# Kernel tuning notes

Measured on AMD Instinct MI355X. Metric: run time of the kernel, lower is better.

Reference implementation:

```python
import jax, jax.numpy as jnp
import numpy as np

EMB = 1024
HEADS = 16
HEADSIZE = EMB // HEADS
LN_EPS = 1e-5


def layernorm(x, w, b):
    # normalize over last dim (headsize)
    mu = jnp.mean(x, axis=-1, keepdims=True)
    var = jnp.var(x, axis=-1, keepdims=True)
    return (x - mu) * jax.lax.rsqrt(var + LN_EPS) * w + b


def setup_inputs() -> dict:
    key = jax.random.key(0)
    ks = jax.random.split(key, 8)
    B, S, C = 2, 2048, 2048
    x = jax.random.normal(ks[0], (B, S, EMB), dtype=jnp.float32)
    context = jax.random.normal(ks[1], (B, C, EMB), dtype=jnp.float32)
    mask = jnp.ones((B, S), dtype=jnp.float32)
    contextMask = jnp.ones((B, C), dtype=jnp.float32)
    s = 0.02
    Wq = jax.random.normal(ks[2], (EMB, EMB), dtype=jnp.float32) * s
    Wk = jax.random.normal(ks[3], (EMB, EMB), dtype=jnp.float32) * s
    Wv = jax.random.normal(ks[4], (EMB, EMB), dtype=jnp.float32) * s
    Wu = jax.random.normal(ks[5], (EMB, EMB), dtype=jnp.float32) * s
    bu = jnp.zeros((EMB,), dtype=jnp.float32)
    qln_w = jnp.ones((HEADSIZE,), dtype=jnp.float32)
    qln_b = jnp.zeros((HEADSIZE,), dtype=jnp.float32)
    kln_w = jnp.ones((HEADSIZE,), dtype=jnp.float32)
    kln_b = jnp.zeros((HEADSIZE,), dtype=jnp.float32)
    return {"x": x, "context": context, "mask": mask, "contextMask": contextMask,
            "Wq": Wq, "Wk": Wk, "Wv": Wv, "Wu": Wu, "bu": bu,
            "qln_w": qln_w, "qln_b": qln_b, "kln_w": kln_w, "kln_b": kln_b}


def reference(x, context, mask, contextMask, Wq, Wk, Wv, Wu, bu, qln_w, qln_b, kln_w, kln_b):
    B, S, E = x.shape
    C = context.shape[1]
    T = S + C
    xc = jnp.concatenate([x, context], axis=1)            # [B, T, E]
    q = (x @ Wq).reshape(B, S, HEADS, HEADSIZE)
    k = (xc @ Wk).reshape(B, T, HEADS, HEADSIZE)
    v = (xc @ Wv).reshape(B, T, HEADS, HEADSIZE)
    q = layernorm(q, qln_w, qln_b)
    k = layernorm(k, kln_w, kln_b)
    scale = E ** 0.25
    q = q / scale
    k = k / scale
    # [B, H, S, T] score matrix (explicitly materialized, as in the original)
    dot = jnp.einsum('bshd,bthd->bhst', q, k)
    mcat = jnp.concatenate([mask, contextMask], axis=1)   # [B, T]
    dotMask = mask[:, None, :, None] * mcat[:, None, None, :]  # [B,1,S,T]
    # hand-rolled masked softmax: softmax(dot*mask) * mask, renormalize
    p = jax.nn.softmax(dot * dotMask, axis=-1) * dotMask
    p = p / (jnp.sum(p, axis=-1, keepdims=True) + 1e-13)
    out = jnp.einsum('bhst,bthd->bshd', p, v).reshape(B, S, E)
    return out @ Wu + bu
```

## Files before the change

### kernel.cpp

```cpp
#include <hip/hip_runtime.h>
#include <hip/hip_bf16.h>
#include <cstdint>

#define B_SZ   2
#define S_LEN  2048
#define C_LEN  2048
#define T_LEN  4096
#define EMB_   1024
#define HEADS_ 16
#define D_     64

typedef __attribute__((ext_vector_type(8))) short bf16x8;
typedef __attribute__((ext_vector_type(4))) float f32x4;
typedef __attribute__((ext_vector_type(16))) float f32x16;
typedef __attribute__((ext_vector_type(2))) float f32x2;

__device__ __forceinline__ unsigned short f2bf(float f) {
    unsigned u = __builtin_bit_cast(unsigned, f);
    u += 0x7fffu + ((u >> 16) & 1u);
    return (unsigned short)(u >> 16);
}
__device__ __forceinline__ float bf2f(unsigned short h) {
    return __builtin_bit_cast(float, (unsigned)h << 16);
}

__global__ void build_xcb_k(const float* __restrict__ x, const float* __restrict__ ctx,
                            unsigned short* __restrict__ xcb) {
    int i = blockIdx.x * blockDim.x + threadIdx.x;
    size_t e8 = (size_t)i * 8;
    int b = (int)(e8 / ((size_t)T_LEN * EMB_));
    size_t rem = e8 % ((size_t)T_LEN * EMB_);
    int t = (int)(rem / EMB_);
    int c = (int)(rem % EMB_);
    const float* src = (t < S_LEN)
        ? &x[((size_t)b * S_LEN + t) * EMB_ + c]
        : &ctx[((size_t)b * C_LEN + (t - S_LEN)) * EMB_ + c];
    float4 v0 = ((const float4*)src)[0];
    float4 v1 = ((const float4*)src)[1];
    uint4 o;
    o.x = (unsigned)f2bf(v0.x) | ((unsigned)f2bf(v0.y) << 16);
    o.y = (unsigned)f2bf(v0.z) | ((unsigned)f2bf(v0.w) << 16);
    o.z = (unsigned)f2bf(v1.x) | ((unsigned)f2bf(v1.y) << 16);
    o.w = (unsigned)f2bf(v1.z) | ((unsigned)f2bf(v1.w) << 16);
    *(uint4*)&xcb[e8] = o;
}

__global__ void mcat_k(const float* __restrict__ mask, const float* __restrict__ cmask,
                       float* __restrict__ Mcat) {
    int i = blockIdx.x * 256 + threadIdx.x;
    int b = i / T_LEN, t = i % T_LEN;
    Mcat[i] = (t < S_LEN) ? mask[(size_t)b * S_LEN + t]
                          : cmask[(size_t)b * C_LEN + (t - S_LEN)];
}

__global__ void wtrans4_k(const float* __restrict__ W0, const float* __restrict__ W1,
                          const float* __restrict__ W2, const float* __restrict__ W3,
                          unsigned short* __restrict__ T0, unsigned short* __restrict__ T1,
                          unsigned short* __restrict__ T2, unsigned short* __restrict__ T3) {
    __shared__ __align__(16) unsigned short tile[64][72];
    int bx = blockIdx.x, by = blockIdx.y, bz = blockIdx.z;
    const float* W = (bz == 0) ? W0 : (bz == 1) ? W1 : (bz == 2) ? W2 : W3;
    unsigned short* WT = (bz == 0) ? T0 : (bz == 1) ? T1 : (bz == 2) ? T2 : T3;
    int tid = threadIdx.x;
#pragma unroll
    for (int r = 0; r < 4; ++r) {
        int idx = tid + r * 256;
        int row = idx >> 4, c4 = idx & 15;
        float4 v = ((const float4*)&W[((size_t)(by * 64 + row)) * EMB_ + bx * 64])[c4];
        tile[row][c4 * 4 + 0] = f2bf(v.x);
        tile[row][c4 * 4 + 1] = f2bf(v.y);
        tile[row][c4 * 4 + 2] = f2bf(v.z);
        tile[row][c4 * 4 + 3] = f2bf(v.w);
    }
    __syncthreads();
#pragma unroll
    for (int r = 0; r < 2; ++r) {
        int idx = tid + r * 256;
        int n = idx >> 3, k8 = idx & 7;
        uint4 o;
        unsigned q[4];
#pragma unroll
        for (int j = 0; j < 4; ++j)
            q[j] = (unsigned)tile[k8 * 8 + 2 * j][n] | ((unsigned)tile[k8 * 8 + 2 * j + 1][n] << 16);
        o.x = q[0]; o.y = q[1]; o.z = q[2]; o.w = q[3];
        *(uint4*)&WT[((size_t)(bx * 64 + n)) * EMB_ + by * 64 + k8 * 8] = o;
    }
}

__global__ __launch_bounds__(256) void gemm_qkv_k(
    const unsigned short* __restrict__ A,
    const unsigned short* __restrict__ Bt,
    unsigned short* __restrict__ Yk,
    unsigned short* __restrict__ Yv,
    unsigned short* __restrict__ Yq) {
    constexpr int KTOT = 1024, NTOT = 1024;
    int nt = blockIdx.x, mt = blockIdx.y;
    if (nt >= 16 && (mt & 31) >= 16) return;
    __shared__ __align__(16) unsigned short As[128 * 32];
    __shared__ __align__(16) unsigned short Bs[128 * 32];
    int in_row0 = mt * 128;
    unsigned short* Cout;
    int col0, out_row0;
    if (nt < 8)       { Cout = Yk; col0 = nt * 128;        out_row0 = mt * 128; }
    else if (nt < 16) { Cout = Yv; col0 = (nt - 8) * 128;  out_row0 = mt * 128; }
    else              { Cout = Yq; col0 = (nt - 16) * 128;
                        out_row0 = (mt >> 5) * 2048 + (mt & 31) * 128; }
    int tid = threadIdx.x, w = tid >> 6, l = tid & 63, l15 = l & 15, lg = l >> 4;
    int wr = (w >> 1) * 64, wc = (w & 1) * 64;

    f32x4 zero4 = {0.f, 0.f, 0.f, 0.f};
    f32x4 acc[4][4];
#pragma unroll
    for (int i = 0; i < 4; ++i)
#pragma unroll
        for (int j = 0; j < 4; ++j) acc[i][j] = zero4;

    for (int k0 = 0; k0 < KTOT; k0 += 32) {
#pragma unroll
        for (int j = 0; j < 2; ++j) {
            int o = tid * 16 + j * 4096;
            int row = o >> 6;
            int ke = (o & 63) >> 1;
            __builtin_amdgcn_global_load_lds(
                (const __attribute__((address_space(1))) void*)&A[(size_t)(in_row0 + row) * KTOT + k0 + ke],
                (__attribute__((address_space(3))) void*)&As[o >> 1], 16, 0, 0);
            __builtin_amdgcn_global_load_lds(
                (const __attribute__((address_space(1))) void*)&Bt[(size_t)(nt * 128 + row) * KTOT + k0 + ke],
                (__attribute__((address_space(3))) void*)&Bs[o >> 1], 16, 0, 0);
        }
        __syncthreads();
        bf16x8 af[4], bf[4];
#pragma unroll
        for (int fr = 0; fr < 4; ++fr)
            af[fr] = *(const bf16x8*)&As[(wr + fr * 16 + l15) * 32 + lg * 8];
#pragma unroll
        for (int fc = 0; fc < 4; ++fc)
            bf[fc] = *(const bf16x8*)&Bs[(wc + fc * 16 + l15) * 32 + lg * 8];
#pragma unroll
        for (int fr = 0; fr < 4; ++fr)
#pragma unroll
            for (int fc = 0; fc < 4; ++fc)
                acc[fr][fc] = __builtin_amdgcn_mfma_f32_16x16x32_bf16(af[fr], bf[fc], acc[fr][fc], 0, 0, 0);
        __syncthreads();
    }
#pragma unroll
    for (int fr = 0; fr < 4; ++fr) {
#pragma unroll
        for (int fc = 0; fc < 4; ++fc) {
            int row = out_row0 + wr + fr * 16 + lg * 4;
            int col = col0 + wc + fc * 16 + l15;
#pragma unroll
            for (int i = 0; i < 4; ++i)
                Cout[(size_t)(row + i) * NTOT + col] = f2bf(acc[fr][fc][i]);
        }
    }
}

template <bool F32OUT>
__global__ __launch_bounds__(256) void gemm_bt_k(
    const unsigned short* __restrict__ A,
    const unsigned short* __restrict__ Bt,
    void* __restrict__ Cout,
    const float* __restrict__ bias,
    int mtiles_per_chunk, int chunk_stride) {
    constexpr int KTOT = 1024, NTOT = 1024;
    __shared__ __align__(16) unsigned short As[128 * 32];
    __shared__ __align__(16) unsigned short Bs[128 * 32];
    int nt = blockIdx.x, mt = blockIdx.y;
    int in_row0 = (mt / mtiles_per_chunk) * chunk_stride + (mt % mtiles_per_chunk) * 128;
    int out_row0 = mt * 128;
    int tid = threadIdx.x, w = tid >> 6, l = tid & 63, l15 = l & 15, lg = l >> 4;
    int wr = (w >> 1) * 64, wc = (w & 1) * 64;

    f32x4 zero4 = {0.f, 0.f, 0.f, 0.f};
    f32x4 acc[4][4];
#pragma unroll
    for (int i = 0; i < 4; ++i)
#pragma unroll
        for (int j = 0; j < 4; ++j) acc[i][j] = zero4;

    for (int k0 = 0; k0 < KTOT; k0 += 32) {
#pragma unroll
        for (int j = 0; j < 2; ++j) {
            int o = tid * 16 + j * 4096;
            int row = o >> 6;
            int ke = (o & 63) >> 1;
            __builtin_amdgcn_global_load_lds(
                (const __attribute__((address_space(1))) void*)&A[(size_t)(in_row0 + row) * KTOT + k0 + ke],
                (__attribute__((address_space(3))) void*)&As[o >> 1], 16, 0, 0);
            __builtin_amdgcn_global_load_lds(
                (const __attribute__((address_space(1))) void*)&Bt[(size_t)(nt * 128 + row) * KTOT + k0 + ke],
                (__attribute__((address_space(3))) void*)&Bs[o >> 1], 16, 0, 0);
        }
        __syncthreads();
        bf16x8 af[4], bf[4];
#pragma unroll
        for (int fr = 0; fr < 4; ++fr)
            af[fr] = *(const bf16x8*)&As[(wr + fr * 16 + l15) * 32 + lg * 8];
#pragma unroll
        for (int fc = 0; fc < 4; ++fc)
            bf[fc] = *(const bf16x8*)&Bs[(wc + fc * 16 + l15) * 32 + lg * 8];
#pragma unroll
        for (int fr = 0; fr < 4; ++fr)
#pragma unroll
            for (int fc = 0; fc < 4; ++fc)
                acc[fr][fc] = __builtin_amdgcn_mfma_f32_16x16x32_bf16(af[fr], bf[fc], acc[fr][fc], 0, 0, 0);
        __syncthreads();
    }
#pragma unroll
    for (int fr = 0; fr < 4; ++fr) {
#pragma unroll
        for (int fc = 0; fc < 4; ++fc) {
            int row = out_row0 + wr + fr * 16 + lg * 4;
            int col = nt * 128 + wc + fc * 16 + l15;
#pragma unroll
            for (int i = 0; i < 4; ++i) {
                float v = acc[fr][fc][i];
                if (F32OUT) {
                    ((float*)Cout)[(size_t)(row + i) * NTOT + col] = v + bias[col];
                } else {
                    ((unsigned short*)Cout)[(size_t)(row + i) * NTOT + col] = f2bf(v);
                }
            }
        }
    }
}

__global__ void ln_head_k(const unsigned short* __restrict__ Y,
                          unsigned short* __restrict__ Out,
                          const float* __restrict__ lw, const float* __restrict__ lb,
                          const float* __restrict__ Mcat,
                          int rows_per_b, float scale) {
    int gw = blockIdx.x * 4 + (threadIdx.x >> 6);
    int lane = threadIdx.x & 63;
    int h = gw % HEADS_;
    int row = gw / HEADS_;
    int b = row / rows_per_b, r = row % rows_per_b;
    float v = bf2f(Y[(size_t)row * EMB_ + h * 64 + lane]);
    float s = v, s2 = v * v;
#pragma unroll
    for (int m = 1; m <= 32; m <<= 1) {
        s += __shfl_xor(s, m);
        s2 += __shfl_xor(s2, m);
    }
    float mu = s * (1.f / 64.f);
    float var = s2 * (1.f / 64.f) - mu * mu;
    float o = (v - mu) * rsqrtf(var + 1e-5f) * lw[lane] + lb[lane];
    float mq = Mcat[(size_t)b * T_LEN + r];
    Out[(((size_t)b * HEADS_ + h) * rows_per_b + r) * 64 + lane] = f2bf(o * scale * mq);
}

__global__ void ln_head_pack_k(const unsigned short* __restrict__ Y,
                               unsigned short* __restrict__ KF,
                               const float* __restrict__ lw, const float* __restrict__ lb,
                               const float* __restrict__ Mcat,
                               float scale) {
    int gw = blockIdx.x * 4 + (threadIdx.x >> 6);
    int lane = threadIdx.x & 63;
    int h = gw % HEADS_;
    int row = gw / HEADS_;
    int b = row / T_LEN, r = row % T_LEN;
    float v = bf2f(Y[(size_t)row * EMB_ + h * 64 + lane]);
    float s = v, s2 = v * v;
#pragma unroll
    for (int m = 1; m <= 32; m <<= 1) {
        s += __shfl_xor(s, m);
        s2 += __shfl_xor(s2, m);
    }
    float mu = s * (1.f / 64.f);
    float var = s2 * (1.f / 64.f) - mu * mu;
    float o = (v - mu) * rsqrtf(var + 1e-5f) * lw[lane] + lb[lane];
    float mt = Mcat[(size_t)b * T_LEN + r];
    int bh = b * HEADS_ + h;
    int kt = r >> 5, l31 = r & 31;
    int sf = lane >> 4, hi = (lane >> 3) & 1, j = lane & 7;
    size_t flat = ((((size_t)bh * 128 + kt) * 4 + sf) * 64 + hi * 32 + l31) * 8 + j;
    KF[flat] = f2bf(o * scale * mt);
}

__global__ void vpack_k(const unsigned short* __restrict__ Yv, unsigned short* __restrict__ VF,
                        const float* __restrict__ Mcat) {
    __shared__ __align__(16) unsigned short tile[64][72];
    __shared__ float msk[64];
    int t0 = blockIdx.x * 64;
    int bh = blockIdx.y;
    int b = bh >> 4, h = bh & 15;
    int tid = threadIdx.x;
    if (tid < 64) msk[tid] = Mcat[(size_t)b * T_LEN + t0 + tid];
#pragma unroll
    for (int rr = 0; rr < 2; ++rr) {
        int idx = tid + rr * 256;
        int row = idx >> 3, c8 = idx & 7;
        *(uint4*)&tile[row][c8 * 8] =
            *(const uint4*)&Yv[((size_t)b * T_LEN + t0 + row) * EMB_ + h * 64 + c8 * 8];
    }
    __syncthreads();
    int f = tid >> 6, l = tid & 63;
    int d = (f >> 1) * 32 + (l & 31);
    int tb = (f & 1) * 16 + 4 * (l >> 5);
#pragma unroll
    for (int ktl = 0; ktl < 2; ++ktl) {
        unsigned short e[8];
#pragma unroll
        for (int j = 0; j < 8; ++j) {
            int tt = ktl * 32 + tb + (j >> 2) * 8 + (j & 3);
            e[j] = f2bf(bf2f(tile[tt][d]) * msk[tt]);
        }
        uint4 o;
        o.x = (unsigned)e[0] | ((unsigned)e[1] << 16);
        o.y = (unsigned)e[2] | ((unsigned)e[3] << 16);
        o.z = (unsigned)e[4] | ((unsigned)e[5] << 16);
        o.w = (unsigned)e[6] | ((unsigned)e[7] << 16);
        size_t kt = (size_t)blockIdx.x * 2 + ktl;
        *(uint4*)&VF[((((size_t)bh * 128 + kt) * 4 + f) * 64 + l) * 8] = o;
    }
}

#define SOFTMAX(SA, LS, PB0, PB1) do {                                            \
    f32x2 e2[8];                                                                  \
    _Pragma("unroll") for (int i_ = 0; i_ < 8; ++i_) {                            \
        e2[i_][0] = __builtin_amdgcn_exp2f(SA[2 * i_]);                           \
        e2[i_][1] = __builtin_amdgcn_exp2f(SA[2 * i_ + 1]);                       \
    }                                                                             \
    {                                                                             \
        float rsA_ = 0.f, rsB_ = 0.f;                                             \
        _Pragma("unroll") for (int i_ = 0; i_ < 8; ++i_) {                        \
            rsA_ = fmaf(e2[i_][0], mt_[2 * i_], rsA_);                            \
            rsB_ = fmaf(e2[i_][1], mt_[2 * i_ + 1], rsB_);                        \
        }                                                                         \
        float rs_ = rsA_ + rsB_;                                                  \
        rs_ += __shfl_xor(rs_, 32);                                               \
        (LS) += rs_;                                                              \
    }                                                                             \
    unsigned pk_[8];                                                              \
    _Pragma("unroll") for (int d_ = 0; d_ < 8; ++d_)                              \
        asm("v_cvt_pk_bf16_f32 %0, %1, %2" : "=v"(pk_[d_])                        \
            : "v"(e2[d_][0]), "v"(e2[d_][1]));                                    \
    { uint4 u0_; u0_.x=pk_[0]; u0_.y=pk_[1]; u0_.z=pk_[2]; u0_.w=pk_[3];          \
      uint4 u1_; u1_.x=pk_[4]; u1_.y=pk_[5]; u1_.z=pk_[6]; u1_.w=pk_[7];          \
      (PB0) = __builtin_bit_cast(bf16x8, u0_);                                    \
      (PB1) = __builtin_bit_cast(bf16x8, u1_); }                                  \
} while (0)

__global__ __launch_bounds__(256) void attn32_k(
    const unsigned short* __restrict__ Q,
    const unsigned short* __restrict__ KF,
    const unsigned short* __restrict__ VF,
    const float* __restrict__ Mcat,
    unsigned short* __restrict__ O) {
    __shared__ __align__(16) unsigned short Ks[2][2048];
    __shared__ __align__(16) unsigned short Vs[2][2048];
    __shared__ float OldsF[4][64][32];
    __shared__ float Llds[4][32];

    int bid = blockIdx.x;
    int xcd = bid & 7, slot = bid >> 3;
    int bh = xcd * 4 + (slot >> 4);
    int qblk = slot & 15;
    int b = bh >> 4, h = bh & 15;
    int tid = threadIdx.x;
    int w = tid >> 6;
    int lane = tid & 63;
    int l31 = lane & 31;
    int hi = lane >> 5;
    int q0 = qblk * 128;
    int qw = q0 + w * 32;

    const unsigned short* KFb_ = KF + (size_t)bh * 262144;
    const unsigned short* VFb_ = VF + (size_t)bh * 262144;
    const float* Mb = Mcat + (size_t)b * T_LEN;

    bf16x8 qf[4];
    {
        const unsigned short* Qp = Q + ((size_t)bh * S_LEN + qw + l31) * 64 + hi * 8;
#pragma unroll
        for (int s = 0; s < 4; ++s) qf[s] = *(const bf16x8*)(Qp + s * 16);
    }

    f32x16 Z16;
#pragma unroll
    for (int i = 0; i < 16; ++i) Z16[i] = 0.f;
    f32x16 acc0 = Z16, acc1 = Z16;
    float lS = 0.f;

#define STAGE(BUF, KT) do {                                                        \
    __builtin_amdgcn_global_load_lds(                                              \
        (const __attribute__((address_space(1))) void*)(KFb_ + (size_t)(KT) * 2048 + tid * 8), \
        (__attribute__((address_space(3))) void*)&Ks[BUF][tid * 8], 16, 0, 0);     \
    __builtin_amdgcn_global_load_lds(                                              \
        (const __attribute__((address_space(1))) void*)(VFb_ + (size_t)(KT) * 2048 + tid * 8), \
        (__attribute__((address_space(3))) void*)&Vs[BUF][tid * 8], 16, 0, 0);     \
} while (0)

    STAGE(0, 0);
    __syncthreads();

    for (int kt = 0; kt < 128; ++kt) {
        int cur = kt & 1;
        if (kt + 1 < 128) STAGE(cur ^ 1, kt + 1);
        const float* mbase = Mb + kt * 32 + 4 * hi;
        float4 mf0 = *(const float4*)(mbase);
        float4 mf1 = *(const float4*)(mbase + 8);
        float4 mf2 = *(const float4*)(mbase + 16);
        float4 mf3 = *(const float4*)(mbase + 24);
        bf16x8 kfr[4], vfr[4];
#pragma unroll
        for (int s = 0; s < 4; ++s) {
            kfr[s] = *(const bf16x8*)&Ks[cur][s * 512 + lane * 8];
            vfr[s] = *(const bf16x8*)&Vs[cur][s * 512 + lane * 8];
        }
        f32x16 sa = Z16;
#pragma unroll
        for (int s = 0; s < 4; ++s)
            sa = __builtin_amdgcn_mfma_f32_32x32x16_bf16(kfr[s], qf[s], sa, 0, 0, 0);
        float mt_[16];
        mt_[0] = mf0.x; mt_[1] = mf0.y; mt_[2]  = mf0.z; mt_[3]  = mf0.w;
        mt_[4] = mf1.x; mt_[5] = mf1.y; mt_[6]  = mf1.z; mt_[7]  = mf1.w;
        mt_[8] = mf2.x; mt_[9] = mf2.y; mt_[10] = mf2.z; mt_[11] = mf2.w;
        mt_[12] = mf3.x; mt_[13] = mf3.y; mt_[14] = mf3.z; mt_[15] = mf3.w;
        bf16x8 p0, p1;
        SOFTMAX(sa, lS, p0, p1);
        acc0 = __builtin_amdgcn_mfma_f32_32x32x16_bf16(vfr[0], p0, acc0, 0, 0, 0);
        acc0 = __builtin_amdgcn_mfma_f32_32x32x16_bf16(vfr[1], p1, acc0, 0, 0, 0);
        acc1 = __builtin_amdgcn_mfma_f32_32x32x16_bf16(vfr[2], p0, acc1, 0, 0, 0);
        acc1 = __builtin_amdgcn_mfma_f32_32x32x16_bf16(vfr[3], p1, acc1, 0, 0, 0);
        __syncthreads();
    }
#undef STAGE

#pragma unroll
    for (int r = 0; r < 16; ++r) {
        int dl = (r & 3) + 8 * (r >> 2) + 4 * hi;
        OldsF[w][dl][l31] = acc0[r];
        OldsF[w][dl + 32][l31] = acc1[r];
    }
    if (hi == 0) Llds[w][l31] = lS;
    __syncthreads();
    {
        int rr = lane >> 1, hf = lane & 1;
        float L = Llds[w][rr];
        float invL = 1.f / (L + 1e-13f);
        float mqz = Mb[q0 + w * 32 + rr];
        invL = (mqz != 0.f) ? invL : 0.f;
        float v_[32];
#pragma unroll
        for (int dd = 0; dd < 32; ++dd)
            v_[dd] = OldsF[w][hf * 32 + dd][rr] * invL;
        unsigned po_[16];
#pragma unroll
        for (int d2 = 0; d2 < 16; ++d2)
            asm("v_cvt_pk_bf16_f32 %0, %1, %2" : "=v"(po_[d2]) : "v"(v_[2*d2]), "v"(v_[2*d2+1]));
        unsigned short* Orow = &O[((size_t)b * S_LEN + qw + rr) * EMB_ + h * 64 + hf * 32];
#pragma unroll
        for (int i = 0; i < 4; ++i) {
            uint4 st;
            st.x = po_[4*i]; st.y = po_[4*i+1]; st.z = po_[4*i+2]; st.w = po_[4*i+3];
            *(uint4*)(Orow + i * 8) = st;
        }
    }
}

extern "C" void kernel_launch(void* const* d_in, const int* in_sizes, int n_in,
                              void* d_out, int out_size, void* d_ws, size_t ws_size,
                              hipStream_t stream) {
    const float* x     = (const float*)d_in[0];
    const float* ctx   = (const float*)d_in[1];
    const float* mask  = (const float*)d_in[2];
    const float* cmask = (const float*)d_in[3];
    const float* Wq    = (const float*)d_in[4];
    const float* Wk    = (const float*)d_in[5];
    const float* Wv    = (const float*)d_in[6];
    const float* Wu    = (const float*)d_in[7];
    const float* bu    = (const float*)d_in[8];
    const float* qlnw  = (const float*)d_in[9];
    const float* qlnb  = (const float*)d_in[10];
    const float* klnw  = (const float*)d_in[11];
    const float* klnb  = (const float*)d_in[12];

    unsigned short* ws = (unsigned short*)d_ws;
    unsigned short* xcb = ws + 0;
    unsigned short* WkT = ws + 8388608;
    unsigned short* WvT = ws + 9437184;
    unsigned short* WqT = ws + 10485760;
    unsigned short* Qb  = ws + 0;
    unsigned short* KFb = ws + 4194304;
    unsigned short* WuT = ws + 12582912;
    unsigned short* Yq  = ws + 13631488;
    unsigned short* Ob  = Yq;
    unsigned short* Yk  = ws + 17825792;
    unsigned short* VFb = Yk;
    unsigned short* Yv  = ws + 26214400;
    float* Mcat         = (float*)(ws + 34603008);

    const float scale = 0.17677669529663687f;
    const float qscale = 0.17677669529663687f * 1.4426950408889634f;

    build_xcb_k<<<4096, 256, 0, stream>>>(x, ctx, xcb);
    mcat_k<<<32, 256, 0, stream>>>(mask, cmask, Mcat);
    wtrans4_k<<<dim3(16, 16, 4), 256, 0, stream>>>(Wk, Wv, Wq, Wu, WkT, WvT, WqT, WuT);

    gemm_qkv_k<<<dim3(24, 64), 256, 0, stream>>>(xcb, WkT, Yk, Yv, Yq);

    ln_head_k<<<16384, 256, 0, stream>>>(Yq, Qb, qlnw, qlnb, Mcat, S_LEN, qscale);
    ln_head_pack_k<<<32768, 256, 0, stream>>>(Yk, KFb, klnw, klnb, Mcat, scale);
    vpack_k<<<dim3(64, 32), 256, 0, stream>>>(Yv, VFb, Mcat);

    attn32_k<<<512, 256, 0, stream>>>(Qb, KFb, VFb, Mcat, Ob);

    gemm_bt_k<true><<<dim3(8, 32), 256, 0, stream>>>(Ob, WuT, d_out, bu, 32, 4096);
}
```

Baseline: 265.9 us.

## Process two key tiles per iteration with doubled LDS staging

The attention main loop now handles two 32-key tiles per iteration instead of one. K/V staging grows to four LDS buffers, so two tiles are prefetched while two are consumed, and there is one barrier per two tiles. The two independent QK^T MFMA chains and softmaxes are interleaved to give the scheduler more independent work. In exchange it uses more registers and LDS, which may reduce occupancy.

```diff
diff --git a/kernel.cpp b/kernel.cpp
--- a/kernel.cpp
+++ b/kernel.cpp
@@ -316,7 +316,7 @@
     }
 }
 
-#define SOFTMAX(SA, LS, PB0, PB1) do {                                            \
+#define SOFTMAX(SA, MT, LS, PB0, PB1) do {                                        \
     f32x2 e2[8];                                                                  \
     _Pragma("unroll") for (int i_ = 0; i_ < 8; ++i_) {                            \
         e2[i_][0] = __builtin_amdgcn_exp2f(SA[2 * i_]);                           \
@@ -325,8 +325,8 @@
     {                                                                             \
         float rsA_ = 0.f, rsB_ = 0.f;                                             \
         _Pragma("unroll") for (int i_ = 0; i_ < 8; ++i_) {                        \
-            rsA_ = fmaf(e2[i_][0], mt_[2 * i_], rsA_);                            \
-            rsB_ = fmaf(e2[i_][1], mt_[2 * i_ + 1], rsB_);                        \
+            rsA_ = fmaf(e2[i_][0], MT[2 * i_], rsA_);                             \
+            rsB_ = fmaf(e2[i_][1], MT[2 * i_ + 1], rsB_);                         \
         }                                                                         \
         float rs_ = rsA_ + rsB_;                                                  \
         rs_ += __shfl_xor(rs_, 32);                                               \
@@ -348,8 +348,8 @@
     const unsigned short* __restrict__ VF,
     const float* __restrict__ Mcat,
     unsigned short* __restrict__ O) {
-    __shared__ __align__(16) unsigned short Ks[2][2048];
-    __shared__ __align__(16) unsigned short Vs[2][2048];
+    __shared__ __align__(16) unsigned short Ks[4][2048];
+    __shared__ __align__(16) unsigned short Vs[4][2048];
     __shared__ float OldsF[4][64][32];
     __shared__ float Llds[4][32];
 
@@ -392,38 +392,59 @@
         (__attribute__((address_space(3))) void*)&Vs[BUF][tid * 8], 16, 0, 0);     \
 } while (0)
 
-    STAGE(0, 0);
+    STAGE(0, 0); STAGE(1, 1);
     __syncthreads();
 
-    for (int kt = 0; kt < 128; ++kt) {
-        int cur = kt & 1;
-        if (kt + 1 < 128) STAGE(cur ^ 1, kt + 1);
-        const float* mbase = Mb + kt * 32 + 4 * hi;
-        float4 mf0 = *(const float4*)(mbase);
-        float4 mf1 = *(const float4*)(mbase + 8);
-        float4 mf2 = *(const float4*)(mbase + 16);
-        float4 mf3 = *(const float4*)(mbase + 24);
-        bf16x8 kfr[4], vfr[4];
+    for (int it = 0; it < 64; ++it) {
+        int base = (it & 1) << 1;
+        int kt0 = it * 2;
+        if (it < 63) {
+            STAGE(base ^ 2, kt0 + 2);
+            STAGE((base ^ 2) + 1, kt0 + 3);
+        }
+        const float* mb0 = Mb + kt0 * 32 + 4 * hi;
+        float4 am0 = *(const float4*)(mb0);
+        float4 am1 = *(const float4*)(mb0 + 8);
+        float4 am2 = *(const float4*)(mb0 + 16);
+        float4 am3 = *(const float4*)(mb0 + 24);
+        float4 bm0 = *(const float4*)(mb0 + 32);
+        float4 bm1 = *(const float4*)(mb0 + 40);
+        float4 bm2 = *(const float4*)(mb0 + 48);
+        float4 bm3 = *(const float4*)(mb0 + 56);
+        bf16x8 kfrA[4], vfrA[4], kfrB[4], vfrB[4];
 #pragma unroll
         for (int s = 0; s < 4; ++s) {
-            kfr[s] = *(const bf16x8*)&Ks[cur][s * 512 + lane * 8];
-            vfr[s] = *(const bf16x8*)&Vs[cur][s * 512 + lane * 8];
-        }
-        f32x16 sa = Z16;
-#pragma unroll
-        for (int s = 0; s < 4; ++s)
-            sa = __builtin_amdgcn_mfma_f32_32x32x16_bf16(kfr[s], qf[s], sa, 0, 0, 0);
-        float mt_[16];
-        mt_[0] = mf0.x; mt_[1] = mf0.y; mt_[2]  = mf0.z; mt_[3]  = mf0.w;
-        mt_[4] = mf1.x; mt_[5] = mf1.y; mt_[6]  = mf1.z; mt_[7]  = mf1.w;
-        mt_[8] = mf2.x; mt_[9] = mf2.y; mt_[10] = mf2.z; mt_[11] = mf2.w;
-        mt_[12] = mf3.x; mt_[13] = mf3.y; mt_[14] = mf3.z; mt_[15] = mf3.w;
-        bf16x8 p0, p1;
-        SOFTMAX(sa, lS, p0, p1);
-        acc0 = __builtin_amdgcn_mfma_f32_32x32x16_bf16(vfr[0], p0, acc0, 0, 0, 0);
-        acc0 = __builtin_amdgcn_mfma_f32_32x32x16_bf16(vfr[1], p1, acc0, 0, 0, 0);
-        acc1 = __builtin_amdgcn_mfma_f32_32x32x16_bf16(vfr[2], p0, acc1, 0, 0, 0);
-        acc1 = __builtin_amdgcn_mfma_f32_32x32x16_bf16(vfr[3], p1, acc1, 0, 0, 0);
+            kfrA[s] = *(const bf16x8*)&Ks[base][s * 512 + lane * 8];
+            vfrA[s] = *(const bf16x8*)&Vs[base][s * 512 + lane * 8];
+            kfrB[s] = *(const bf16x8*)&Ks[base + 1][s * 512 + lane * 8];
+            vfrB[s] = *(const bf16x8*)&Vs[base + 1][s * 512 + lane * 8];
+        }
+        f32x16 saA = Z16, saB = Z16;
+#pragma unroll
+        for (int s = 0; s < 4; ++s) {
+            saA = __builtin_amdgcn_mfma_f32_32x32x16_bf16(kfrA[s], qf[s], saA, 0, 0, 0);
+            saB = __builtin_amdgcn_mfma_f32_32x32x16_bf16(kfrB[s], qf[s], saB, 0, 0, 0);
+        }
+        float mtA_[16], mtB_[16];
+        mtA_[0] = am0.x; mtA_[1] = am0.y; mtA_[2]  = am0.z; mtA_[3]  = am0.w;
+        mtA_[4] = am1.x; mtA_[5] = am1.y; mtA_[6]  = am1.z; mtA_[7]  = am1.w;
+        mtA_[8] = am2.x; mtA_[9] = am2.y; mtA_[10] = am2.z; mtA_[11] = am2.w;
+        mtA_[12] = am3.x; mtA_[13] = am3.y; mtA_[14] = am3.z; mtA_[15] = am3.w;
+        mtB_[0] = bm0.x; mtB_[1] = bm0.y; mtB_[2]  = bm0.z; mtB_[3]  = bm0.w;
+        mtB_[4] = bm1.x; mtB_[5] = bm1.y; mtB_[6]  = bm1.z; mtB_[7]  = bm1.w;
+        mtB_[8] = bm2.x; mtB_[9] = bm2.y; mtB_[10] = bm2.z; mtB_[11] = bm2.w;
+        mtB_[12] = bm3.x; mtB_[13] = bm3.y; mtB_[14] = bm3.z; mtB_[15] = bm3.w;
+        bf16x8 p0A, p1A, p0B, p1B;
+        SOFTMAX(saA, mtA_, lS, p0A, p1A);
+        SOFTMAX(saB, mtB_, lS, p0B, p1B);
+        acc0 = __builtin_amdgcn_mfma_f32_32x32x16_bf16(vfrA[0], p0A, acc0, 0, 0, 0);
+        acc1 = __builtin_amdgcn_mfma_f32_32x32x16_bf16(vfrA[2], p0A, acc1, 0, 0, 0);
+        acc0 = __builtin_amdgcn_mfma_f32_32x32x16_bf16(vfrA[1], p1A, acc0, 0, 0, 0);
+        acc1 = __builtin_amdgcn_mfma_f32_32x32x16_bf16(vfrA[3], p1A, acc1, 0, 0, 0);
+        acc0 = __builtin_amdgcn_mfma_f32_32x32x16_bf16(vfrB[0], p0B, acc0, 0, 0, 0);
+        acc1 = __builtin_amdgcn_mfma_f32_32x32x16_bf16(vfrB[2], p0B, acc1, 0, 0, 0);
+        acc0 = __builtin_amdgcn_mfma_f32_32x32x16_bf16(vfrB[1], p1B, acc0, 0, 0, 0);
+        acc1 = __builtin_amdgcn_mfma_f32_32x32x16_bf16(vfrB[3], p1B, acc1, 0, 0, 0);
         __syncthreads();
     }
 #undef STAGE
```

After: 239.1 us. 1.11x faster.

## Deepen K/V LDS ring to 8 tiles and process tiles in pairs

Applied to the files above, without the earlier changes.

The attention loop now stages four 32-key tiles per iteration into an 8-slot LDS ring, so it prefetches four tiles ahead instead of one. Each iteration processes two pairs of tiles, issuing two independent QK MFMA chains and two softmaxes before the PV MFMAs. This cuts barriers per key by four and gives the scheduler more independent work to hide latency. The epilogue buffers are unioned with the ring to limit LDS growth, but the ring still grows to 64KB, which may reduce occupancy and raises register pressure.

```diff
diff --git a/kernel.cpp b/kernel.cpp
--- a/kernel.cpp
+++ b/kernel.cpp
@@ -316,7 +316,7 @@
     }
 }
 
-#define SOFTMAX(SA, LS, PB0, PB1) do {                                            \
+#define SOFTMAX(SA, MT, LS, PB0, PB1) do {                                        \
     f32x2 e2[8];                                                                  \
     _Pragma("unroll") for (int i_ = 0; i_ < 8; ++i_) {                            \
         e2[i_][0] = __builtin_amdgcn_exp2f(SA[2 * i_]);                           \
@@ -325,8 +325,8 @@
     {                                                                             \
         float rsA_ = 0.f, rsB_ = 0.f;                                             \
         _Pragma("unroll") for (int i_ = 0; i_ < 8; ++i_) {                        \
-            rsA_ = fmaf(e2[i_][0], mt_[2 * i_], rsA_);                            \
-            rsB_ = fmaf(e2[i_][1], mt_[2 * i_ + 1], rsB_);                        \
+            rsA_ = fmaf(e2[i_][0], MT[2 * i_], rsA_);                             \
+            rsB_ = fmaf(e2[i_][1], MT[2 * i_ + 1], rsB_);                         \
         }                                                                         \
         float rs_ = rsA_ + rsB_;                                                  \
         rs_ += __shfl_xor(rs_, 32);                                               \
@@ -342,16 +342,24 @@
       (PB1) = __builtin_bit_cast(bf16x8, u1_); }                                  \
 } while (0)
 
+union AttnSmem {
+    struct {
+        unsigned short Ks[8][2048];
+        unsigned short Vs[8][2048];
+    } ring;
+    struct {
+        float OldsF[4][64][32];
+        float Llds[4][32];
+    } epi;
+};
+
 __global__ __launch_bounds__(256) void attn32_k(
     const unsigned short* __restrict__ Q,
     const unsigned short* __restrict__ KF,
     const unsigned short* __restrict__ VF,
     const float* __restrict__ Mcat,
     unsigned short* __restrict__ O) {
-    __shared__ __align__(16) unsigned short Ks[2][2048];
-    __shared__ __align__(16) unsigned short Vs[2][2048];
-    __shared__ float OldsF[4][64][32];
-    __shared__ float Llds[4][32];
+    __shared__ __align__(16) AttnSmem smem;
 
     int bid = blockIdx.x;
     int xcd = bid & 7, slot = bid >> 3;
@@ -386,66 +394,93 @@
 #define STAGE(BUF, KT) do {                                                        \
     __builtin_amdgcn_global_load_lds(                                              \
         (const __attribute__((address_space(1))) void*)(KFb_ + (size_t)(KT) * 2048 + tid * 8), \
-        (__attribute__((address_space(3))) void*)&Ks[BUF][tid * 8], 16, 0, 0);     \
+        (__attribute__((address_space(3))) void*)&smem.ring.Ks[BUF][tid * 8], 16, 0, 0); \
     __builtin_amdgcn_global_load_lds(                                              \
         (const __attribute__((address_space(1))) void*)(VFb_ + (size_t)(KT) * 2048 + tid * 8), \
-        (__attribute__((address_space(3))) void*)&Vs[BUF][tid * 8], 16, 0, 0);     \
+        (__attribute__((address_space(3))) void*)&smem.ring.Vs[BUF][tid * 8], 16, 0, 0); \
 } while (0)
 
-    STAGE(0, 0);
+#define PAIR(B0, MTBASE) do {                                                      \
+    const float* mbp_ = (MTBASE);                                                  \
+    float4 am0 = *(const float4*)(mbp_);                                           \
+    float4 am1 = *(const float4*)(mbp_ + 8);                                       \
+    float4 am2 = *(const float4*)(mbp_ + 16);                                      \
+    float4 am3 = *(const float4*)(mbp_ + 24);                                      \
+    float4 bm0 = *(const float4*)(mbp_ + 32);                                      \
+    float4 bm1 = *(const float4*)(mbp_ + 40);                                      \
+    float4 bm2 = *(const float4*)(mbp_ + 48);                                      \
+    float4 bm3 = *(const float4*)(mbp_ + 56);                                      \
+    bf16x8 kfrA[4], vfrA[4], kfrB[4], vfrB[4];                                     \
+    _Pragma("unroll") for (int s_ = 0; s_ < 4; ++s_) {                             \
+        kfrA[s_] = *(const bf16x8*)&smem.ring.Ks[B0][s_ * 512 + lane * 8];         \
+        vfrA[s_] = *(const bf16x8*)&smem.ring.Vs[B0][s_ * 512 + lane * 8];         \
+        kfrB[s_] = *(const bf16x8*)&smem.ring.Ks[(B0) + 1][s_ * 512 + lane * 8];   \
+        vfrB[s_] = *(const bf16x8*)&smem.ring.Vs[(B0) + 1][s_ * 512 + lane * 8];   \
+    }                                                                              \
+    f32x16 saA = Z16, saB = Z16;                                                   \
+    _Pragma("unroll") for (int s_ = 0; s_ < 4; ++s_) {                             \
+        saA = __builtin_amdgcn_mfma_f32_32x32x16_bf16(kfrA[s_], qf[s_], saA, 0, 0, 0); \
+        saB = __builtin_amdgcn_mfma_f32_32x32x16_bf16(kfrB[s_], qf[s_], saB, 0, 0, 0); \
+    }                                                                              \
+    float mtA_[16], mtB_[16];                                                      \
+    mtA_[0] = am0.x; mtA_[1] = am0.y; mtA_[2]  = am0.z; mtA_[3]  = am0.w;          \
+    mtA_[4] = am1.x; mtA_[5] = am1.y; mtA_[6]  = am1.z; mtA_[7]  = am1.w;          \
+    mtA_[8] = am2.x; mtA_[9] = am2.y; mtA_[10] = am2.z; mtA_[11] = am2.w;          \
+    mtA_[12] = am3.x; mtA_[13] = am3.y; mtA_[14] = am3.z; mtA_[15] = am3.w;        \
+    mtB_[0] = bm0.x; mtB_[1] = bm0.y; mtB_[2]  = bm0.z; mtB_[3]  = bm0.w;          \
+    mtB_[4] = bm1.x; mtB_[5] = bm1.y; mtB_[6]  = bm1.z; mtB_[7]  = bm1.w;          \
+    mtB_[8] = bm2.x; mtB_[9] = bm2.y; mtB_[10] = bm2.z; mtB_[11] = bm2.w;          \
+    mtB_[12] = bm3.x; mtB_[13] = bm3.y; mtB_[14] = bm3.z; mtB_[15] = bm3.w;        \
+    bf16x8 p0A, p1A, p0B, p1B;                                                     \
+    SOFTMAX(saA, mtA_, lS, p0A, p1A);                                              \
+    SOFTMAX(saB, mtB_, lS, p0B, p1B);                                              \
+    acc0 = __builtin_amdgcn_mfma_f32_32x32x16_bf16(vfrA[0], p0A, acc0, 0, 0, 0);   \
+    acc1 = __builtin_amdgcn_mfma_f32_32x32x16_bf16(vfrA[2], p0A, acc1, 0, 0, 0);   \
+    acc0 = __builtin_amdgcn_mfma_f32_32x32x16_bf16(vfrA[1], p1A, acc0, 0, 0, 0);   \
+    acc1 = __builtin_amdgcn_mfma_f32_32x32x16_bf16(vfrA[3], p1A, acc1, 0, 0, 0);   \
+    acc0 = __builtin_amdgcn_mfma_f32_32x32x16_bf16(vfrB[0], p0B, acc0, 0, 0, 0);   \
+    acc1 = __builtin_amdgcn_mfma_f32_32x32x16_bf16(vfrB[2], p0B, acc1, 0, 0, 0);   \
+    acc0 = __builtin_amdgcn_mfma_f32_32x32x16_bf16(vfrB[1], p1B, acc0, 0, 0, 0);   \
+    acc1 = __builtin_amdgcn_mfma_f32_32x32x16_bf16(vfrB[3], p1B, acc1, 0, 0, 0);   \
+} while (0)
+
+    STAGE(0, 0); STAGE(1, 1); STAGE(2, 2); STAGE(3, 3);
     __syncthreads();
 
-    for (int kt = 0; kt < 128; ++kt) {
-        int cur = kt & 1;
-        if (kt + 1 < 128) STAGE(cur ^ 1, kt + 1);
-        const float* mbase = Mb + kt * 32 + 4 * hi;
-        float4 mf0 = *(const float4*)(mbase);
-        float4 mf1 = *(const float4*)(mbase + 8);
-        float4 mf2 = *(const float4*)(mbase + 16);
-        float4 mf3 = *(const float4*)(mbase + 24);
-        bf16x8 kfr[4], vfr[4];
-#pragma unroll
-        for (int s = 0; s < 4; ++s) {
-            kfr[s] = *(const bf16x8*)&Ks[cur][s * 512 + lane * 8];
-            vfr[s] = *(const bf16x8*)&Vs[cur][s * 512 + lane * 8];
-        }
-        f32x16 sa = Z16;
-#pragma unroll
-        for (int s = 0; s < 4; ++s)
-            sa = __builtin_amdgcn_mfma_f32_32x32x16_bf16(kfr[s], qf[s], sa, 0, 0, 0);
-        float mt_[16];
-        mt_[0] = mf0.x; mt_[1] = mf0.y; mt_[2]  = mf0.z; mt_[3]  = mf0.w;
-        mt_[4] = mf1.x; mt_[5] = mf1.y; mt_[6]  = mf1.z; mt_[7]  = mf1.w;
-        mt_[8] = mf2.x; mt_[9] = mf2.y; mt_[10] = mf2.z; mt_[11] = mf2.w;
-        mt_[12] = mf3.x; mt_[13] = mf3.y; mt_[14] = mf3.z; mt_[15] = mf3.w;
-        bf16x8 p0, p1;
-        SOFTMAX(sa, lS, p0, p1);
-        acc0 = __builtin_amdgcn_mfma_f32_32x32x16_bf16(vfr[0], p0, acc0, 0, 0, 0);
-        acc0 = __builtin_amdgcn_mfma_f32_32x32x16_bf16(vfr[1], p1, acc0, 0, 0, 0);
-        acc1 = __builtin_amdgcn_mfma_f32_32x32x16_bf16(vfr[2], p0, acc1, 0, 0, 0);
-        acc1 = __builtin_amdgcn_mfma_f32_32x32x16_bf16(vfr[3], p1, acc1, 0, 0, 0);
+    for (int it = 0; it < 32; ++it) {
+        int base = (it & 1) << 2;
+        int kt0 = it * 4;
+        if (it < 31) {
+            int ob = base ^ 4;
+            STAGE(ob, kt0 + 4); STAGE(ob + 1, kt0 + 5);
+            STAGE(ob + 2, kt0 + 6); STAGE(ob + 3, kt0 + 7);
+        }
+        const float* mb0 = Mb + kt0 * 32 + 4 * hi;
+        PAIR(base, mb0);
+        PAIR(base + 2, mb0 + 64);
         __syncthreads();
     }
+#undef PAIR
 #undef STAGE
 
 #pragma unroll
     for (int r = 0; r < 16; ++r) {
         int dl = (r & 3) + 8 * (r >> 2) + 4 * hi;
-        OldsF[w][dl][l31] = acc0[r];
-        OldsF[w][dl + 32][l31] = acc1[r];
-    }
-    if (hi == 0) Llds[w][l31] = lS;
+        smem.epi.OldsF[w][dl][l31] = acc0[r];
+        smem.epi.OldsF[w][dl + 32][l31] = acc1[r];
+    }
+    if (hi == 0) smem.epi.Llds[w][l31] = lS;
     __syncthreads();
     {
         int rr = lane >> 1, hf = lane & 1;
-        float L = Llds[w][rr];
+        float L = smem.epi.Llds[w][rr];
         float invL = 1.f / (L + 1e-13f);
         float mqz = Mb[q0 + w * 32 + rr];
         invL = (mqz != 0.f) ? invL : 0.f;
         float v_[32];
 #pragma unroll
         for (int dd = 0; dd < 32; ++dd)
-            v_[dd] = OldsF[w][hf * 32 + dd][rr] * invL;
+            v_[dd] = smem.epi.OldsF[w][hf * 32 + dd][rr] * invL;
         unsigned po_[16];
 #pragma unroll
         for (int d2 = 0; d2 < 16; ++d2)
```

Result: faster. 245.2 us (-7.8%).
